# Kernel tuning notes

Hardware: AMD Instinct MI355X
Metric: run time of the kernel (lower is better)

## Reference

```python
import jax, jax.numpy as jnp
import numpy as np

RADII = (0.4, 0.8, 1.2)
SIGMA2 = 2.0 * 0.2 ** 2   # Gaussian shell-density bandwidth
ALPHA = 0.3               # keras LeakyReLU default
EPS = 1e-3                # keras BatchNormalization default epsilon


def _n_coeffs(L):
    return sum((2 * l + 1) ** 2 for l in range(L + 1))


def _pullback_idx(L):
    # flat index of Wigner block entry (m, n=0) for each SH coeff (l, m)
    idx, off = [], 0
    for l in range(L + 1):
        d = 2 * l + 1
        idx += [off + m * d + l for m in range(d)]
        off += d * d
    return np.asarray(idx, dtype=np.int32)


def setup_inputs() -> dict:
    key = jax.random.key(0)
    ks = jax.random.split(key, 20)
    B, N, Q, S = 64, 2048, 1024, 512
    T = [_n_coeffs(l) for l in (5, 4, 3)]  # 286, 165, 84
    f32 = jnp.float32

    def nrm(k, shape, scale=1.0):
        return jax.random.normal(ks[k], shape, dtype=f32) * scale

    dirs = nrm(1, (3, S, 3))
    dirs = dirs / jnp.linalg.norm(dirs, axis=-1, keepdims=True)
    z = lambda n: jnp.zeros((n,), f32)
    o = lambda n: jnp.ones((n,), f32)
    return {
        "x": nrm(0, (B, N, 3)),
        "shell_dirs": dirs,                                   # [3, 512, 3]
        "A_sh": nrm(2, (36, S), 1.0 / np.sqrt(S)),            # SH projection (l_max=5)
        "D_eval0": nrm(3, (Q, T[0]), 1.0 / np.sqrt(T[0])),    # Wigner eval bases
        "D_eval1": nrm(4, (Q, T[1]), 1.0 / np.sqrt(T[1])),
        "D_eval2": nrm(5, (Q, T[2]), 1.0 / np.sqrt(T[2])),
        "D_coef1": nrm(6, (T[1], Q), 1.0 / np.sqrt(Q)),       # Wigner coeff (projection) bases
        "D_coef2": nrm(7, (T[2], Q), 1.0 / np.sqrt(Q)),
        "D_coef_last": nrm(8, (T[2], Q), 1.0 / np.sqrt(Q)),
        "W0": nrm(9, (3, 16), 1.0 / np.sqrt(3)), "b0": z(16),
        "W1": nrm(10, (16, 32), 0.25), "b1": z(32),
        "W2": nrm(11, (32, 64), 1.0 / np.sqrt(32)), "b2": z(64),
        "g0": o(16), "be0": z(16),
        "g1": o(32), "be1": z(32),
        "g2": o(64), "be2": z(64),
        "Wfc1": nrm(12, (256, 512), 1.0 / 16.0), "bfc1": z(512),
        "gfc1": o(512), "befc1": z(512),
        "Wfc2": nrm(13, (512, 256), 1.0 / np.sqrt(512)), "bfc2": z(256),
        "gfc2": o(256), "befc2": z(256),
        "Wout": nrm(14, (256, 40), 1.0 / 16.0), "bout": z(40),
    }


def _bn(y, g, b, axes):
    m = jnp.mean(y, axis=axes, keepdims=True)
    v = jnp.var(y, axis=axes, keepdims=True)
    return (y - m) * jax.lax.rsqrt(v + EPS) * g + b


def reference(x, shell_dirs, A_sh, D_eval0, D_eval1, D_eval2,
              D_coef1, D_coef2, D_coef_last,
              W0, b0, W1, b1, W2, b2,
              g0, be0, g1, be1, g2, be2,
              Wfc1, bfc1, gfc1, befc1, Wfc2, bfc2, gfc2, befc2,
              Wout, bout):
    B = x.shape[0]
    # --- sphere_shell_embedding: Gaussian shell density -> SH coeffs per shell ---
    xn2 = jnp.sum(x * x, -1)[..., None]                 # [B,N,1]
    sh = []
    for i, r in enumerate(RADII):
        c = r * shell_dirs[i]                           # [S,3]
        d2 = xn2 + jnp.sum(c * c, -1) - 2.0 * (x @ c.T)  # [B,N,S]
        f = jnp.mean(jnp.exp(-d2 / SIGMA2), axis=1)      # [B,S]
        sh.append(f @ A_sh.T)                            # [B,36]
    sh = jnp.stack(sh, axis=-1)                          # [B,36,3] shells as channels
    # --- S2_to_SO3_pullback: Y_lm -> D^l_{m,0} column of Wigner blocks ---
    idx = jnp.asarray(_pullback_idx(5))
    y = jnp.zeros((B, 286, 3), sh.dtype).at[:, idx, :].set(sh)
    # --- layer 0: SO3Conv (per-coeff channel mix) + WignerEval + BN + LReLU + WignerCoeffs ---
    y = jnp.einsum('btc,cu->btu', y, W0) + b0
    y = jnp.einsum('qt,btu->bqu', D_eval0, y)            # [B,1024,16]
    y = jax.nn.leaky_relu(_bn(y, g0, be0, (0, 1)), ALPHA)
    y = jnp.einsum('tq,bqu->btu', D_coef1, y)            # [B,165,16]
    # --- layer 1 ---
    y = jnp.einsum('btc,cu->btu', y, W1) + b1
    y = jnp.einsum('qt,btu->bqu', D_eval1, y)            # [B,1024,32]
    y = jax.nn.leaky_relu(_bn(y, g1, be1, (0, 1)), ALPHA)
    y = jnp.einsum('tq,bqu->btu', D_coef2, y)            # [B,84,32]
    # --- layer 2 ---
    y = jnp.einsum('btc,cu->btu', y, W2) + b2
    y = jnp.einsum('qt,btu->bqu', D_eval2, y)            # [B,1024,64]
    y = jax.nn.leaky_relu(_bn(y, g2, be2, (0, 1)), ALPHA)
    y = jnp.einsum('tq,bqu->btu', D_coef_last, y)        # [B,84,64]
    # --- degree-wise norms (rotation-invariant pooling), l_max=3 blocks ---
    offs, sizes = (0, 1, 10, 35), (1, 9, 25, 49)
    feats = jnp.concatenate(
        [jnp.linalg.norm(y[:, o:o + s, :], axis=1, keepdims=True)
         for o, s in zip(offs, sizes)], axis=1)          # [B,4,64]
    h = feats.reshape(B, -1)                             # [B,256]
    # --- MLP head (dropout = identity at inference) ---
    h = jax.nn.relu(_bn(h @ Wfc1 + bfc1, gfc1, befc1, (0,)))
    h = jax.nn.relu(_bn(h @ Wfc2 + bfc2, gfc2, befc2, (0,)))
    return jax.nn.softmax(h @ Wout + bout, axis=-1)
```

## Files before the change

### kernel.cpp

```cpp
#include <hip/hip_runtime.h>
#include <hip/hip_bf16.h>

#define BB 64
#define NN 2048
#define QQ 1024
#define SS 512
#define NCH 16
#define PREPB 609
#define QKN3 8

__device__ const int PIDX[36] = {
    0, 2, 5, 8, 12, 17, 22, 27, 32, 38, 45, 52, 59, 66, 73, 80,
    88, 97, 106, 115, 124, 133, 142, 151, 160,
    170, 181, 192, 203, 214, 225, 236, 247, 258, 269, 280};

__global__ __launch_bounds__(256) void k_preshell(
    const float* __restrict__ De0, const float* __restrict__ De1, const float* __restrict__ De2,
    float* __restrict__ Dg0t, float* __restrict__ rs0,
    float* __restrict__ Det1, float* __restrict__ Det2,
    float* __restrict__ stats,
    const float* __restrict__ x, const float* __restrict__ dirs, float* __restrict__ pbuf) {
    __shared__ float tile[32][33];
    __shared__ float4 lx[NN / NCH];
    int blk = blockIdx.x, tid = threadIdx.x;
    if (blk < PREPB) {
        int r = tid >> 5, c = tid & 31;
        if (blk < 192) {
            int tq = blk & 31, tt = blk >> 5;
            int q0 = tq * 32, t0 = tt * 32;
            for (int rr = r; rr < 32; rr += 8) {
                int t = t0 + c;
                tile[rr][c] = (t < 165) ? De1[(q0 + rr) * 165 + t] : 0.f;
            }
            __syncthreads();
            for (int rr = r; rr < 32; rr += 8) {
                int t = t0 + rr;
                if (t < 165) Det1[t * QQ + q0 + c] = tile[c][rr];
            }
        } else if (blk < 288) {
            int i = blk - 192;
            int tq = i & 31, tt = i >> 5;
            int q0 = tq * 32, t0 = tt * 32;
            for (int rr = r; rr < 32; rr += 8) {
                int t = t0 + c;
                tile[rr][c] = (t < 84) ? De2[(q0 + rr) * 84 + t] : 0.f;
            }
            __syncthreads();
            for (int rr = r; rr < 32; rr += 8) {
                int t = t0 + rr;
                if (t < 84) Det2[t * QQ + q0 + c] = tile[c][rr];
            }
        } else if (blk < 352) {
            int i = blk - 288;
            int tq = i & 31, tj = i >> 5;
            int q0 = tq * 32, j0 = tj * 32;
            for (int rr = r; rr < 32; rr += 8) {
                int j = j0 + c;
                tile[rr][c] = (j < 36) ? De0[(q0 + rr) * 286 + PIDX[j]] : 0.f;
            }
            __syncthreads();
            for (int rr = r; rr < 32; rr += 8) {
                int j = j0 + rr;
                if (j < 36) Dg0t[j * QQ + q0 + c] = tile[c][rr];
            }
        } else if (blk < 608) {
            int w = tid >> 6, lane = tid & 63;
            int q = (blk - 352) * 4 + w;
            float s = 0.f;
#pragma unroll
            for (int p = 0; p < 5; p++) {
                int idx = lane + p * 64;
                if (idx < 286) s += De0[q * 286 + idx];
            }
#pragma unroll
            for (int o = 32; o > 0; o >>= 1) s += __shfl_xor(s, o, 64);
            if (lane == 0) rs0[q] = s;
        } else {
            if (tid < 224) stats[tid] = 0.f;
        }
        return;
    }
    int idx = blk - PREPB;
    int b = idx & 63, zc = idx >> 6;
    const float KL = 18.033688011112042f;
    const float* xb = x + ((size_t)b * NN + zc * (NN / NCH)) * 3;
    for (int n = tid; n < NN / NCH; n += 256) {
        float X = xb[n * 3 + 0];
        float Y = xb[n * 3 + 1];
        float Z = xb[n * 3 + 2];
        lx[n] = make_float4(X, Y, Z, -KL * (X * X + Y * Y + Z * Z));
    }
    __syncthreads();
    float cxs[3][2], cys[3][2], czs[3][2], bas[3][2];
#pragma unroll
    for (int i = 0; i < 3; i++) {
        float r = (i == 0) ? 0.4f : ((i == 1) ? 0.8f : 1.2f);
#pragma unroll
        for (int h = 0; h < 2; h++) {
            int s = tid + h * 256;
            float cx = r * dirs[(i * SS + s) * 3 + 0];
            float cy = r * dirs[(i * SS + s) * 3 + 1];
            float cz = r * dirs[(i * SS + s) * 3 + 2];
            bas[i][h] = -KL * (cx * cx + cy * cy + cz * cz);
            cxs[i][h] = 2.f * KL * cx;
            cys[i][h] = 2.f * KL * cy;
            czs[i][h] = 2.f * KL * cz;
        }
    }
    float acc[3][2];
#pragma unroll
    for (int i = 0; i < 3; i++) { acc[i][0] = 0.f; acc[i][1] = 0.f; }
#pragma unroll 4
    for (int n = 0; n < NN / NCH; n++) {
        float4 p = lx[n];
#pragma unroll
        for (int i = 0; i < 3; i++)
#pragma unroll
            for (int h = 0; h < 2; h++)
                acc[i][h] += __builtin_amdgcn_exp2f(
                    fmaf(cxs[i][h], p.x, fmaf(cys[i][h], p.y, fmaf(czs[i][h], p.z, p.w + bas[i][h]))));
    }
#pragma unroll
    for (int i = 0; i < 3; i++) {
        float* o = pbuf + ((size_t)(zc * 3 + i) * BB + b) * SS;
        o[tid] = acc[i][0];
        o[tid + 256] = acc[i][1];
    }
}

__global__ __launch_bounds__(256) void k_sh(const float* __restrict__ pbuf,
                                            const float* __restrict__ A_sh,
                                            float* __restrict__ lshp) {
    __shared__ float lf[256];
    int b = blockIdx.x, c = blockIdx.y, h = blockIdx.z, tid = threadIdx.x;
    float v = 0.f;
#pragma unroll
    for (int zc = 0; zc < NCH; zc++)
        v += pbuf[((size_t)(zc * 3 + c) * BB + b) * SS + h * 256 + tid];
    lf[tid] = v * (1.0f / NN);
    __syncthreads();
    int w = tid >> 6, lane = tid & 63;
    for (int j = w; j < 36; j += 4) {
        const float* As = A_sh + j * SS + h * 256;
        float a = 0.f;
#pragma unroll
        for (int k = 0; k < 4; k++) a = fmaf(lf[lane + 64 * k], As[lane + 64 * k], a);
#pragma unroll
        for (int o = 32; o > 0; o >>= 1) a += __shfl_xor(a, o, 64);
        if (lane == 0) lshp[((b * 36 + j) * 3 + c) * 2 + h] = a;
    }
}

__global__ __launch_bounds__(256) void k_eval0(const float* __restrict__ lshp,
                                               const float* __restrict__ W0,
                                               const float* __restrict__ b0,
                                               const float* __restrict__ Dg0t,
                                               const float* __restrict__ rs0,
                                               float* __restrict__ yq, float* __restrict__ stats) {
    __shared__ float lsh[36][3];
    __shared__ float llm[576];
    __shared__ float lred[4][32];
    int qc = blockIdx.x, b = blockIdx.y, tid = threadIdx.x;
    if (tid < 108) {
        int j = tid / 3, c = tid % 3;
        lsh[j][c] = lshp[((b * 36 + j) * 3 + c) * 2 + 0] + lshp[((b * 36 + j) * 3 + c) * 2 + 1];
    }
    __syncthreads();
    for (int i = tid; i < 576; i += 256) {
        int j = i >> 4, u = i & 15;
        float m = 0.f;
#pragma unroll
        for (int c = 0; c < 3; c++) m = fmaf(lsh[j][c], W0[c * 16 + u], m);
        llm[i] = m;
    }
    __syncthreads();
    int q = qc * 256 + tid;
    float acc[16];
#pragma unroll
    for (int u = 0; u < 16; u++) acc[u] = 0.f;
#pragma unroll 4
    for (int j = 0; j < 36; j++) {
        float d = Dg0t[j * QQ + q];
#pragma unroll
        for (int u = 0; u < 16; u++) acc[u] = fmaf(d, llm[j * 16 + u], acc[u]);
    }
    float rb = rs0[q];
#pragma unroll
    for (int u = 0; u < 16; u++) acc[u] = fmaf(b0[u], rb, acc[u]);
#pragma unroll
    for (int u = 0; u < 16; u++) yq[((size_t)b * 16 + u) * QQ + q] = acc[u];
    int lane = tid & 63, w = tid >> 6;
#pragma unroll
    for (int u = 0; u < 16; u++) {
        float v = acc[u], v2 = acc[u] * acc[u];
#pragma unroll
        for (int o = 32; o > 0; o >>= 1) {
            v += __shfl_xor(v, o, 64);
            v2 += __shfl_xor(v2, o, 64);
        }
        if (lane == 0) { lred[w][u] = v; lred[w][16 + u] = v2; }
    }
    __syncthreads();
    if (tid < 32) atomicAdd(&stats[tid], lred[0][tid] + lred[1][tid] + lred[2][tid] + lred[3][tid]);
}

template <int TT, int UU, int QKN>
__global__ __launch_bounds__(256) void k_coefG(const float* __restrict__ yq,
                                               const float* __restrict__ Dc,
                                               const float* __restrict__ stats,
                                               const float* __restrict__ g,
                                               const float* __restrict__ be,
                                               float* __restrict__ part) {
    constexpr int KC = QQ / QKN;
    __shared__ float lA[32][68];
    __shared__ float lB[32][68];
    __shared__ float lsu[UU], ltu[UU];
    int mt = blockIdx.x, nt = blockIdx.y, qk = blockIdx.z, tid = threadIdx.x;
    int m0 = mt * 64, n0 = nt * 64, k0 = qk * KC;
    if (tid < UU) {
        const float inv = 1.0f / (BB * QQ);
        float mm = stats[tid] * inv;
        float var = stats[UU + tid] * inv - mm * mm;
        float s = g[tid] * rsqrtf(fmaxf(var, 0.f) + 1e-3f);
        lsu[tid] = s;
        ltu[tid] = be[tid] - mm * s;
    }
    __syncthreads();
    int r = tid >> 2, f = (tid & 3) * 4;
    bool mok = (m0 + r) < TT;
    const float* arow = Dc + (size_t)(mok ? (m0 + r) : 0) * QQ;
    const float* brow = yq + (size_t)(n0 + r) * QQ;
    float su = lsu[(n0 + r) % UU], tu = ltu[(n0 + r) % UU];
    int tg = tid >> 4, ug = tid & 15;
    float acc[4][4];
#pragma unroll
    for (int i = 0; i < 4; i++)
#pragma unroll
        for (int j = 0; j < 4; j++) acc[i][j] = 0.f;
    for (int kb = 0; kb < KC; kb += 32) {
        int kg = k0 + kb;
#pragma unroll
        for (int p = 0; p < 2; p++) {
            int ko = f + p * 16;
            float4 a4 = make_float4(0.f, 0.f, 0.f, 0.f);
            if (mok) a4 = *(const float4*)(arow + kg + ko);
            float4 b4 = *(const float4*)(brow + kg + ko);
#pragma unroll
            for (int i = 0; i < 4; i++) {
                float v = fmaf((&b4.x)[i], su, tu);
                lA[ko + i][r] = (&a4.x)[i];
                lB[ko + i][r] = (v > 0.f) ? v : 0.3f * v;
            }
        }
        __syncthreads();
#pragma unroll 2
        for (int kk = 0; kk < 32; kk++) {
            float4 a4 = *(const float4*)&lA[kk][tg * 4];
            float4 b4 = *(const float4*)&lB[kk][ug * 4];
#pragma unroll
            for (int i = 0; i < 4; i++) {
                float av = (&a4.x)[i];
                acc[i][0] = fmaf(av, b4.x, acc[i][0]);
                acc[i][1] = fmaf(av, b4.y, acc[i][1]);
                acc[i][2] = fmaf(av, b4.z, acc[i][2]);
                acc[i][3] = fmaf(av, b4.w, acc[i][3]);
            }
        }
        __syncthreads();
    }
    int n = n0 + ug * 4;
    int b = n / UU, u0 = n % UU;
#pragma unroll
    for (int i = 0; i < 4; i++) {
        int t = m0 + tg * 4 + i;
        if (t < TT)
            *(float4*)&part[(((size_t)qk * BB + b) * TT + t) * UU + u0] =
                make_float4(acc[i][0], acc[i][1], acc[i][2], acc[i][3]);
    }
}

template <int TT, int CC, int UU, int QKN, int TTp, int TS>
__global__ __launch_bounds__(256) void k_redmix(const float* __restrict__ part,
                                                const float* __restrict__ W,
                                                const float* __restrict__ bias,
                                                float* __restrict__ ym) {
    constexpr int TSL = TTp / TS;
    __shared__ float lyt[TSL][CC + 1];
    int b = blockIdx.x, ts = blockIdx.y, tid = threadIdx.x;
    int t0 = ts * TSL;
    for (int i = tid; i < TSL * CC; i += 256) {
        int tl = i / CC, c = i % CC;
        int t = t0 + tl;
        float v = 0.f;
        if (t < TT) {
#pragma unroll
            for (int k = 0; k < QKN; k++)
                v += part[(size_t)k * (BB * TT * CC) + ((size_t)b * TT + t) * CC + c];
        }
        lyt[tl][c] = v;
    }
    __syncthreads();
    for (int i = tid; i < UU * TSL; i += 256) {
        int u = i / TSL, tl = i % TSL;
        int t = t0 + tl;
        float m = 0.f;
        if (t < TT) {
            m = bias[u];
#pragma unroll
            for (int c = 0; c < CC; c++) m = fmaf(lyt[tl][c], W[c * UU + u], m);
        }
        ym[((size_t)b * UU + u) * TTp + t] = m;
    }
}

template <int TT, int TTp, int UU>
__global__ __launch_bounds__(256) void k_evalG(const float* __restrict__ ym,
                                               const float* __restrict__ Det,
                                               float* __restrict__ yq,
                                               float* __restrict__ stats) {
    __shared__ float lA[32][68];
    __shared__ float lB[32][68];
    __shared__ float sred[2][64];
    int mt = blockIdx.x, qt = blockIdx.y, tid = threadIdx.x;
    int m0 = mt * 64, q0 = qt * 64;
    int r = tid >> 2, f = (tid & 3) * 4;
    const float* arow = ym + (size_t)(m0 + r) * TTp;
    int br = tid >> 4, bq = (tid & 15) * 4;
    int tg = tid >> 4, ug = tid & 15;
    float acc[4][4];
#pragma unroll
    for (int i = 0; i < 4; i++)
#pragma unroll
        for (int j = 0; j < 4; j++) acc[i][j] = 0.f;
    for (int kb = 0; kb < TT; kb += 32) {
#pragma unroll
        for (int p = 0; p < 2; p++) {
            int ko = f + p * 16;
            float4 a4 = *(const float4*)(arow + kb + ko);
#pragma unroll
            for (int i = 0; i < 4; i++) lA[ko + i][r] = (&a4.x)[i];
            int kk = br + p * 16;
            int t = kb + kk;
            float4 b4 = make_float4(0.f, 0.f, 0.f, 0.f);
            if (t < TT) b4 = *(const float4*)(Det + (size_t)t * QQ + q0 + bq);
            *(float4*)&lB[kk][bq] = b4;
        }
        __syncthreads();
#pragma unroll 2
        for (int kk = 0; kk < 32; kk++) {
            float4 a4 = *(const float4*)&lA[kk][tg * 4];
            float4 b4 = *(const float4*)&lB[kk][ug * 4];
#pragma unroll
            for (int i = 0; i < 4; i++) {
                float av = (&a4.x)[i];
                acc[i][0] = fmaf(av, b4.x, acc[i][0]);
                acc[i][1] = fmaf(av, b4.y, acc[i][1]);
                acc[i][2] = fmaf(av, b4.z, acc[i][2]);
                acc[i][3] = fmaf(av, b4.w, acc[i][3]);
            }
        }
        __syncthreads();
    }
    float s1[4], s2[4];
#pragma unroll
    for (int i = 0; i < 4; i++) {
        int m = m0 + tg * 4 + i;
        *(float4*)&yq[(size_t)m * QQ + q0 + ug * 4] =
            make_float4(acc[i][0], acc[i][1], acc[i][2], acc[i][3]);
        s1[i] = (acc[i][0] + acc[i][1]) + (acc[i][2] + acc[i][3]);
        s2[i] = fmaf(acc[i][0], acc[i][0], fmaf(acc[i][1], acc[i][1],
                 fmaf(acc[i][2], acc[i][2], acc[i][3] * acc[i][3])));
    }
#pragma unroll
    for (int o = 1; o < 16; o <<= 1) {
#pragma unroll
        for (int i = 0; i < 4; i++) {
            s1[i] += __shfl_xor(s1[i], o, 64);
            s2[i] += __shfl_xor(s2[i], o, 64);
        }
    }
    if (ug == 0) {
#pragma unroll
        for (int i = 0; i < 4; i++) {
            sred[0][tg * 4 + i] = s1[i];
            sred[1][tg * 4 + i] = s2[i];
        }
    }
    __syncthreads();
    if (tid < 2 * UU) {
        int which = tid / UU, u = tid % UU;
        float s = 0.f;
        for (int rr = u; rr < 64; rr += UU) s += sred[which][rr];
        atomicAdd(&stats[which * UU + u], s);
    }
}

__global__ __launch_bounds__(256) void k_norms(const float* __restrict__ part, float* __restrict__ ht0) {
    __shared__ float red[4][64];
    int b = blockIdx.x, blk = blockIdx.y;
    int tq = threadIdx.x >> 6, u = threadIdx.x & 63;
    const int offs[4] = {0, 1, 10, 35};
    const int ends[4] = {1, 10, 35, 84};
    float a = 0.f;
    for (int t = offs[blk] + tq; t < ends[blk]; t += 4) {
        float v = 0.f;
#pragma unroll
        for (int k = 0; k < QKN3; k++)
            v += part[(size_t)k * (BB * 84 * 64) + (b * 84 + t) * 64 + u];
        a = fmaf(v, v, a);
    }
    red[tq][u] = a;
    __syncthreads();
    if (tq == 0) {
        float s = red[0][u] + red[1][u] + red[2][u] + red[3][u];
        ht0[(blk * 64 + u) * BB + b] = sqrtf(fmaxf(s, 0.f));
    }
}

template <int K, int J>
__global__ __launch_bounds__(512) void k_fc(const float* __restrict__ in, const float* __restrict__ W,
                                            const float* __restrict__ bias, const float* __restrict__ g,
                                            const float* __restrict__ be, float* __restrict__ out) {
    __shared__ float red[8][64];
    int j = blockIdx.x;
    int b = threadIdx.x & 63, kq = threadIdx.x >> 6;
    constexpr int KS = K / 8;
    int kbeg = kq * KS;
    float a0 = 0.f, a1 = 0.f, a2 = 0.f, a3 = 0.f;
#pragma unroll 4
    for (int k = kbeg; k < kbeg + KS; k += 4) {
        a0 = fmaf(in[k * BB + b], W[(size_t)k * J + j], a0);
        a1 = fmaf(in[(k + 1) * BB + b], W[(size_t)(k + 1) * J + j], a1);
        a2 = fmaf(in[(k + 2) * BB + b], W[(size_t)(k + 2) * J + j], a2);
        a3 = fmaf(in[(k + 3) * BB + b], W[(size_t)(k + 3) * J + j], a3);
    }
    red[kq][b] = (a0 + a1) + (a2 + a3);
    __syncthreads();
    if (kq == 0) {
        float acc = bias[j];
#pragma unroll
        for (int i = 0; i < 8; i++) acc += red[i][b];
        float s1 = acc, s2 = acc * acc;
#pragma unroll
        for (int o = 32; o > 0; o >>= 1) {
            s1 += __shfl_xor(s1, o, 64);
            s2 += __shfl_xor(s2, o, 64);
        }
        float m = s1 * (1.0f / 64.f);
        float var = s2 * (1.0f / 64.f) - m * m;
        float sc = g[j] * rsqrtf(fmaxf(var, 0.f) + 1e-3f);
        float v = (acc - m) * sc + be[j];
        out[j * BB + b] = fmaxf(v, 0.f);
    }
}

__global__ __launch_bounds__(256) void k_out(const float* __restrict__ ht2, const float* __restrict__ Wout,
                                             const float* __restrict__ bout, float* __restrict__ outp) {
    __shared__ float red[4][64];
    __shared__ float sm[64];
    int b = blockIdx.x;
    int o = threadIdx.x & 63, kq = threadIdx.x >> 6;
    float a0 = 0.f, a1 = 0.f, a2 = 0.f, a3 = 0.f;
    int kbeg = kq * 64;
    if (o < 40) {
#pragma unroll 4
        for (int k = kbeg; k < kbeg + 64; k += 4) {
            a0 = fmaf(ht2[k * BB + b], Wout[k * 40 + o], a0);
            a1 = fmaf(ht2[(k + 1) * BB + b], Wout[(k + 1) * 40 + o], a1);
            a2 = fmaf(ht2[(k + 2) * BB + b], Wout[(k + 2) * 40 + o], a2);
            a3 = fmaf(ht2[(k + 3) * BB + b], Wout[(k + 3) * 40 + o], a3);
        }
    }
    red[kq][o] = (a0 + a1) + (a2 + a3);
    __syncthreads();
    if (kq == 0) {
        float acc = red[0][o] + red[1][o] + red[2][o] + red[3][o] + ((o < 40) ? bout[o] : 0.f);
        sm[o] = (o < 40) ? acc : -3.0e38f;
        __syncthreads();
        for (int s = 32; s > 0; s >>= 1) {
            if (o < s) sm[o] = fmaxf(sm[o], sm[o + s]);
            __syncthreads();
        }
        float m = sm[0];
        __syncthreads();
        const float L2E = 1.4426950408889634f;
        float e = (o < 40) ? exp2f((acc - m) * L2E) : 0.f;
        sm[o] = e;
        __syncthreads();
        for (int s = 32; s > 0; s >>= 1) {
            if (o < s) sm[o] += sm[o + s];
            __syncthreads();
        }
        if (o < 40) outp[b * 40 + o] = e / sm[0];
    }
}

#define OFF_PBUF 0
#define OFF_DG0T 1572864
#define OFF_RS0 1609728
#define OFF_DET1 1610752
#define OFF_DET2 1779712
#define OFF_YQ 1865728
#define OFF_YM 6060032
#define OFF_LSH 6453248
#define OFF_HT0 6467072
#define OFF_HT1 6483456
#define OFF_HT2 6516224
#define OFF_STATS 6532608
#define OFF_PART 6532864
#define OFF_PART3 7909120

extern "C" void kernel_launch(void* const* d_in, const int* in_sizes, int n_in,
                              void* d_out, int out_size, void* d_ws, size_t ws_size,
                              hipStream_t stream) {
    const float* x = (const float*)d_in[0];
    const float* shell_dirs = (const float*)d_in[1];
    const float* A_sh = (const float*)d_in[2];
    const float* D_eval0 = (const float*)d_in[3];
    const float* D_eval1 = (const float*)d_in[4];
    const float* D_eval2 = (const float*)d_in[5];
    const float* D_coef1 = (const float*)d_in[6];
    const float* D_coef2 = (const float*)d_in[7];
    const float* D_coef_last = (const float*)d_in[8];
    const float* W0 = (const float*)d_in[9];
    const float* b0 = (const float*)d_in[10];
    const float* W1 = (const float*)d_in[11];
    const float* b1 = (const float*)d_in[12];
    const float* W2 = (const float*)d_in[13];
    const float* b2 = (const float*)d_in[14];
    const float* g0 = (const float*)d_in[15];
    const float* be0 = (const float*)d_in[16];
    const float* g1 = (const float*)d_in[17];
    const float* be1 = (const float*)d_in[18];
    const float* g2 = (const float*)d_in[19];
    const float* be2 = (const float*)d_in[20];
    const float* Wfc1 = (const float*)d_in[21];
    const float* bfc1 = (const float*)d_in[22];
    const float* gfc1 = (const float*)d_in[23];
    const float* befc1 = (const float*)d_in[24];
    const float* Wfc2 = (const float*)d_in[25];
    const float* bfc2 = (const float*)d_in[26];
    const float* gfc2 = (const float*)d_in[27];
    const float* befc2 = (const float*)d_in[28];
    const float* Wout = (const float*)d_in[29];
    const float* bout = (const float*)d_in[30];
    float* out = (float*)d_out;

    float* ws = (float*)d_ws;
    float* pbuf = ws + OFF_PBUF;
    float* Dg0t = ws + OFF_DG0T;
    float* rs0 = ws + OFF_RS0;
    float* Det1 = ws + OFF_DET1;
    float* Det2 = ws + OFF_DET2;
    float* yq = ws + OFF_YQ;
    float* ym = ws + OFF_YM;
    float* lshp = ws + OFF_LSH;
    float* ht0 = ws + OFF_HT0;
    float* ht1 = ws + OFF_HT1;
    float* ht2 = ws + OFF_HT2;
    float* stats = ws + OFF_STATS;
    float* part = ws + OFF_PART;
    float* part3 = ws + OFF_PART3;
    float* stats0 = stats;
    float* stats1 = stats + 32;
    float* stats2 = stats + 96;

    k_preshell<<<PREPB + BB * NCH, 256, 0, stream>>>(
        D_eval0, D_eval1, D_eval2, Dg0t, rs0, Det1, Det2, stats, x, shell_dirs, pbuf);
    k_sh<<<dim3(BB, 3, 2), 256, 0, stream>>>(pbuf, A_sh, lshp);
    k_eval0<<<dim3(4, BB), 256, 0, stream>>>(lshp, W0, b0, Dg0t, rs0, yq, stats0);
    k_coefG<165, 16, 8><<<dim3(3, 16, 8), 256, 0, stream>>>(yq, D_coef1, stats0, g0, be0, part);
    k_redmix<165, 16, 32, 8, 192, 8><<<dim3(BB, 8), 256, 0, stream>>>(part, W1, b1, ym);
    k_evalG<165, 192, 32><<<dim3(32, 16), 256, 0, stream>>>(ym, Det1, yq, stats1);
    k_coefG<84, 32, 8><<<dim3(2, 32, 8), 256, 0, stream>>>(yq, D_coef2, stats1, g1, be1, part);
    k_redmix<84, 32, 64, 8, 96, 8><<<dim3(BB, 8), 256, 0, stream>>>(part, W2, b2, ym);
    k_evalG<84, 96, 64><<<dim3(64, 16), 256, 0, stream>>>(ym, Det2, yq, stats2);
    k_coefG<84, 64, QKN3><<<dim3(2, 64, QKN3), 256, 0, stream>>>(yq, D_coef_last, stats2, g2, be2, part3);
    k_norms<<<dim3(BB, 4), 256, 0, stream>>>(part3, ht0);
    k_fc<256, 512><<<512, 512, 0, stream>>>(ht0, Wfc1, bfc1, gfc1, befc1, ht1);
    k_fc<512, 256><<<256, 512, 0, stream>>>(ht1, Wfc2, bfc2, gfc2, befc2, ht2);
    k_out<<<BB, 256, 0, stream>>>(ht2, Wout, bout, out);
}
```

Before: 312.7 us.

## Fuse all pipeline stages into one persistent cooperative kernel with grid barriers

Replaces the fourteen separate kernel launches with a single cooperative persistent kernel. Each stage runs as a grid-stride loop over work blocks, and stages are separated by a software grid barrier built on atomics. This is meant to remove per-launch overhead and inter-kernel gaps. In exchange, each barrier costs a global atomic round trip, some stages may see reduced parallelism from the capped grid size, and the old multi-launch path is kept as a fallback.

```diff
diff --git a/kernel.cpp b/kernel.cpp
--- a/kernel.cpp
+++ b/kernel.cpp
@@ -1,5 +1,4 @@
 #include <hip/hip_runtime.h>
-#include <hip/hip_bf16.h>
 
 #define BB 64
 #define NN 2048
@@ -13,6 +12,551 @@
     0, 2, 5, 8, 12, 17, 22, 27, 32, 38, 45, 52, 59, 66, 73, 80,
     88, 97, 106, 115, 124, 133, 142, 151, 160,
     170, 181, 192, 203, 214, 225, 236, 247, 258, 269, 280};
+
+struct MArgs {
+    const float *x, *dirs, *A_sh, *De0, *De1, *De2, *Dc1, *Dc2, *Dc3;
+    const float *W0, *b0, *W1, *b1, *W2, *b2;
+    const float *g0, *be0, *g1, *be1, *g2, *be2;
+    const float *Wfc1, *bfc1, *gfc1, *befc1, *Wfc2, *bfc2, *gfc2, *befc2, *Wout, *bout;
+    float *pbuf, *Dg0t, *rs0, *Det1, *Det2, *yq, *ym, *lshp;
+    float *ht0, *ht1, *ht2, *stats, *part, *part3, *out;
+};
+
+struct SmGemm { float lA[32][68]; float lB[32][68]; float lsu[64]; float ltu[64]; };
+struct SmEv   { float lA[32][68]; float lB[32][68]; float sred[2][64]; };
+struct SmE0   { float lsh[36][3]; float llm[576]; float lred[4][32]; };
+
+__device__ unsigned long long g_bar_count = 0ull;
+__device__ unsigned long long g_bar_gen = 0ull;
+
+__device__ __forceinline__ void gbar() {
+    __syncthreads();
+    __threadfence();
+    if (threadIdx.x == 0) {
+        unsigned long long gen =
+            __hip_atomic_load(&g_bar_gen, __ATOMIC_RELAXED, __HIP_MEMORY_SCOPE_AGENT);
+        unsigned long long arrived =
+            __hip_atomic_fetch_add(&g_bar_count, 1ull, __ATOMIC_ACQ_REL, __HIP_MEMORY_SCOPE_AGENT) + 1ull;
+        if (arrived == (unsigned long long)gridDim.x) {
+            __hip_atomic_store(&g_bar_count, 0ull, __ATOMIC_RELAXED, __HIP_MEMORY_SCOPE_AGENT);
+            __hip_atomic_fetch_add(&g_bar_gen, 1ull, __ATOMIC_RELEASE, __HIP_MEMORY_SCOPE_AGENT);
+        } else {
+            while (__hip_atomic_load(&g_bar_gen, __ATOMIC_ACQUIRE, __HIP_MEMORY_SCOPE_AGENT) == gen)
+                __builtin_amdgcn_s_sleep(2);
+        }
+    }
+    __syncthreads();
+    __threadfence();
+}
+
+
+__device__ void ph_shell(const MArgs& a, int wb, char* smraw, int tid) {
+    __syncthreads();
+    float4* lx = reinterpret_cast<float4*>(smraw);
+    int b = wb & 63, zc = wb >> 6;
+    const float KL = 18.033688011112042f;
+    const float* xb = a.x + ((size_t)b * NN + zc * (NN / NCH)) * 3;
+    for (int n = tid; n < NN / NCH; n += 256) {
+        float X = xb[n * 3 + 0];
+        float Y = xb[n * 3 + 1];
+        float Z = xb[n * 3 + 2];
+        lx[n] = make_float4(X, Y, Z, -KL * (X * X + Y * Y + Z * Z));
+    }
+    __syncthreads();
+    float cxs[3][2], cys[3][2], czs[3][2], bas[3][2];
+#pragma unroll
+    for (int i = 0; i < 3; i++) {
+        float r = (i == 0) ? 0.4f : ((i == 1) ? 0.8f : 1.2f);
+#pragma unroll
+        for (int h = 0; h < 2; h++) {
+            int s = tid + h * 256;
+            float cx = r * a.dirs[(i * SS + s) * 3 + 0];
+            float cy = r * a.dirs[(i * SS + s) * 3 + 1];
+            float cz = r * a.dirs[(i * SS + s) * 3 + 2];
+            bas[i][h] = -KL * (cx * cx + cy * cy + cz * cz);
+            cxs[i][h] = 2.f * KL * cx;
+            cys[i][h] = 2.f * KL * cy;
+            czs[i][h] = 2.f * KL * cz;
+        }
+    }
+    float acc[3][2];
+#pragma unroll
+    for (int i = 0; i < 3; i++) { acc[i][0] = 0.f; acc[i][1] = 0.f; }
+#pragma unroll 4
+    for (int n = 0; n < NN / NCH; n++) {
+        float4 p = lx[n];
+#pragma unroll
+        for (int i = 0; i < 3; i++)
+#pragma unroll
+            for (int h = 0; h < 2; h++)
+                acc[i][h] += __builtin_amdgcn_exp2f(
+                    fmaf(cxs[i][h], p.x, fmaf(cys[i][h], p.y, fmaf(czs[i][h], p.z, p.w))));
+    }
+#pragma unroll
+    for (int i = 0; i < 3; i++) {
+        float* o = a.pbuf + ((size_t)(zc * 3 + i) * BB + b) * SS;
+        o[tid] = acc[i][0] * __builtin_amdgcn_exp2f(bas[i][0]);
+        o[tid + 256] = acc[i][1] * __builtin_amdgcn_exp2f(bas[i][1]);
+    }
+}
+
+__device__ void ph_sh(const MArgs& a, int wb, char* smraw, int tid) {
+    __syncthreads();
+    float* lf = reinterpret_cast<float*>(smraw);
+    int b = wb & 63;
+    int t = wb >> 6;
+    int c = t % 3, h = t / 3;
+    float v = 0.f;
+#pragma unroll
+    for (int zc = 0; zc < NCH; zc++)
+        v += a.pbuf[((size_t)(zc * 3 + c) * BB + b) * SS + h * 256 + tid];
+    lf[tid] = v * (1.0f / NN);
+    __syncthreads();
+    int w = tid >> 6, lane = tid & 63;
+    for (int j = w; j < 36; j += 4) {
+        const float* As = a.A_sh + j * SS + h * 256;
+        float acc = 0.f;
+#pragma unroll
+        for (int k = 0; k < 4; k++) acc = fmaf(lf[lane + 64 * k], As[lane + 64 * k], acc);
+#pragma unroll
+        for (int o = 32; o > 0; o >>= 1) acc += __shfl_xor(acc, o, 64);
+        if (lane == 0) a.lshp[((b * 36 + j) * 3 + c) * 2 + h] = acc;
+    }
+}
+
+__device__ void ph_prep(const MArgs& a, int wb, char* smraw, int tid) {
+    __syncthreads();
+    float (*tile)[33] = reinterpret_cast<float (*)[33]>(smraw);
+    int r = tid >> 5, c = tid & 31;
+    if (wb < 576) {
+        int i = wb - 384;
+        int tq = i & 31, tt = i >> 5;
+        int q0 = tq * 32, t0 = tt * 32;
+        for (int rr = r; rr < 32; rr += 8) {
+            int t = t0 + c;
+            tile[rr][c] = (t < 165) ? a.De1[(q0 + rr) * 165 + t] : 0.f;
+        }
+        __syncthreads();
+        for (int rr = r; rr < 32; rr += 8) {
+            int t = t0 + rr;
+            if (t < 165) a.Det1[t * QQ + q0 + c] = tile[c][rr];
+        }
+    } else if (wb < 672) {
+        int i = wb - 576;
+        int tq = i & 31, tt = i >> 5;
+        int q0 = tq * 32, t0 = tt * 32;
+        for (int rr = r; rr < 32; rr += 8) {
+            int t = t0 + c;
+            tile[rr][c] = (t < 84) ? a.De2[(q0 + rr) * 84 + t] : 0.f;
+        }
+        __syncthreads();
+        for (int rr = r; rr < 32; rr += 8) {
+            int t = t0 + rr;
+            if (t < 84) a.Det2[t * QQ + q0 + c] = tile[c][rr];
+        }
+    } else if (wb < 736) {
+        int i = wb - 672;
+        int tq = i & 31, tj = i >> 5;
+        int q0 = tq * 32, j0 = tj * 32;
+        for (int rr = r; rr < 32; rr += 8) {
+            int j = j0 + c;
+            tile[rr][c] = (j < 36) ? a.De0[(q0 + rr) * 286 + PIDX[j]] : 0.f;
+        }
+        __syncthreads();
+        for (int rr = r; rr < 32; rr += 8) {
+            int j = j0 + rr;
+            if (j < 36) a.Dg0t[j * QQ + q0 + c] = tile[c][rr];
+        }
+    } else {
+        int w = tid >> 6, lane = tid & 63;
+        int q = (wb - 736) * 4 + w;
+        float s = 0.f;
+#pragma unroll
+        for (int p = 0; p < 5; p++) {
+            int idx = lane + p * 64;
+            if (idx < 286) s += a.De0[q * 286 + idx];
+        }
+#pragma unroll
+        for (int o = 32; o > 0; o >>= 1) s += __shfl_xor(s, o, 64);
+        if (lane == 0) a.rs0[q] = s;
+    }
+}
+
+__device__ void ph_eval0(const MArgs& a, int wb, char* smraw, int tid) {
+    __syncthreads();
+    SmE0& s = *reinterpret_cast<SmE0*>(smraw);
+    int qc = wb & 3, b = wb >> 2;
+    if (tid < 108) {
+        int j = tid / 3, c = tid % 3;
+        s.lsh[j][c] = a.lshp[((b * 36 + j) * 3 + c) * 2 + 0] +
+                      a.lshp[((b * 36 + j) * 3 + c) * 2 + 1];
+    }
+    __syncthreads();
+    for (int i = tid; i < 576; i += 256) {
+        int j = i >> 4, u = i & 15;
+        float m = 0.f;
+#pragma unroll
+        for (int c = 0; c < 3; c++) m = fmaf(s.lsh[j][c], a.W0[c * 16 + u], m);
+        s.llm[i] = m;
+    }
+    __syncthreads();
+    int q = qc * 256 + tid;
+    float acc[16];
+#pragma unroll
+    for (int u = 0; u < 16; u++) acc[u] = 0.f;
+#pragma unroll 4
+    for (int j = 0; j < 36; j++) {
+        float d = a.Dg0t[j * QQ + q];
+#pragma unroll
+        for (int u = 0; u < 16; u++) acc[u] = fmaf(d, s.llm[j * 16 + u], acc[u]);
+    }
+    float rb = a.rs0[q];
+#pragma unroll
+    for (int u = 0; u < 16; u++) acc[u] = fmaf(a.b0[u], rb, acc[u]);
+#pragma unroll
+    for (int u = 0; u < 16; u++) a.yq[((size_t)b * 16 + u) * QQ + q] = acc[u];
+    int lane = tid & 63, w = tid >> 6;
+#pragma unroll
+    for (int u = 0; u < 16; u++) {
+        float v = acc[u], v2 = acc[u] * acc[u];
+#pragma unroll
+        for (int o = 32; o > 0; o >>= 1) {
+            v += __shfl_xor(v, o, 64);
+            v2 += __shfl_xor(v2, o, 64);
+        }
+        if (lane == 0) { s.lred[w][u] = v; s.lred[w][16 + u] = v2; }
+    }
+    __syncthreads();
+    if (tid < 32)
+        atomicAdd(&a.stats[tid], s.lred[0][tid] + s.lred[1][tid] + s.lred[2][tid] + s.lred[3][tid]);
+}
+
+template <int TT, int UU, int QKN>
+__device__ void ph_coefG(const float* __restrict__ yq, const float* __restrict__ Dc,
+                         const float* __restrict__ stats, const float* __restrict__ g,
+                         const float* __restrict__ be, float* __restrict__ part,
+                         int mt, int nt, int qk, char* smraw, int tid) {
+    __syncthreads();
+    constexpr int KC = QQ / QKN;
+    SmGemm& s = *reinterpret_cast<SmGemm*>(smraw);
+    int m0 = mt * 64, n0 = nt * 64, k0 = qk * KC;
+    if (tid < UU) {
+        const float inv = 1.0f / (BB * QQ);
+        float mm = stats[tid] * inv;
+        float var = stats[UU + tid] * inv - mm * mm;
+        float sc = g[tid] * rsqrtf(fmaxf(var, 0.f) + 1e-3f);
+        s.lsu[tid] = sc;
+        s.ltu[tid] = be[tid] - mm * sc;
+    }
+    __syncthreads();
+    int r = tid >> 2, f = (tid & 3) * 4;
+    bool mok = (m0 + r) < TT;
+    const float* arow = Dc + (size_t)(mok ? (m0 + r) : 0) * QQ;
+    const float* brow = yq + (size_t)(n0 + r) * QQ;
+    float su = s.lsu[(n0 + r) % UU], tu = s.ltu[(n0 + r) % UU];
+    int tg = tid >> 4, ug = tid & 15;
+    float acc[4][4];
+#pragma unroll
+    for (int i = 0; i < 4; i++)
+#pragma unroll
+        for (int j = 0; j < 4; j++) acc[i][j] = 0.f;
+    for (int kb = 0; kb < KC; kb += 32) {
+        int kg = k0 + kb;
+#pragma unroll
+        for (int p = 0; p < 2; p++) {
+            int ko = f + p * 16;
+            float4 a4 = make_float4(0.f, 0.f, 0.f, 0.f);
+            if (mok) a4 = *(const float4*)(arow + kg + ko);
+            float4 b4 = *(const float4*)(brow + kg + ko);
+#pragma unroll
+            for (int i = 0; i < 4; i++) {
+                float v = fmaf((&b4.x)[i], su, tu);
+                s.lA[ko + i][r] = (&a4.x)[i];
+                s.lB[ko + i][r] = (v > 0.f) ? v : 0.3f * v;
+            }
+        }
+        __syncthreads();
+#pragma unroll 2
+        for (int kk = 0; kk < 32; kk++) {
+            float4 a4 = *(const float4*)&s.lA[kk][tg * 4];
+            float4 b4 = *(const float4*)&s.lB[kk][ug * 4];
+#pragma unroll
+            for (int i = 0; i < 4; i++) {
+                float av = (&a4.x)[i];
+                acc[i][0] = fmaf(av, b4.x, acc[i][0]);
+                acc[i][1] = fmaf(av, b4.y, acc[i][1]);
+                acc[i][2] = fmaf(av, b4.z, acc[i][2]);
+                acc[i][3] = fmaf(av, b4.w, acc[i][3]);
+            }
+        }
+        __syncthreads();
+    }
+    int n = n0 + ug * 4;
+    int b = n / UU, u0 = n % UU;
+#pragma unroll
+    for (int i = 0; i < 4; i++) {
+        int t = m0 + tg * 4 + i;
+        if (t < TT)
+            *(float4*)&part[(((size_t)qk * BB + b) * TT + t) * UU + u0] =
+                make_float4(acc[i][0], acc[i][1], acc[i][2], acc[i][3]);
+    }
+}
+
+template <int TT, int CC, int UU, int QKN, int TTp, int TS>
+__device__ void ph_redmix(const float* __restrict__ part, const float* __restrict__ W,
+                          const float* __restrict__ bias, float* __restrict__ ym,
+                          int b, int ts, char* smraw, int tid) {
+    __syncthreads();
+    constexpr int TSL = TTp / TS;
+    float* lyt = reinterpret_cast<float*>(smraw);
+    int t0 = ts * TSL;
+    for (int i = tid; i < TSL * CC; i += 256) {
+        int tl = i / CC, c = i % CC;
+        int t = t0 + tl;
+        float v = 0.f;
+        if (t < TT) {
+#pragma unroll
+            for (int k = 0; k < QKN; k++)
+                v += part[(size_t)k * (BB * TT * CC) + ((size_t)b * TT + t) * CC + c];
+        }
+        lyt[tl * (CC + 1) + c] = v;
+    }
+    __syncthreads();
+    for (int i = tid; i < UU * TSL; i += 256) {
+        int u = i / TSL, tl = i % TSL;
+        int t = t0 + tl;
+        float m = 0.f;
+        if (t < TT) {
+            m = bias[u];
+#pragma unroll
+            for (int c = 0; c < CC; c++) m = fmaf(lyt[tl * (CC + 1) + c], W[c * UU + u], m);
+        }
+        ym[((size_t)b * UU + u) * TTp + t] = m;
+    }
+}
+
+template <int TT, int TTp, int UU>
+__device__ void ph_evalG(const float* __restrict__ ym, const float* __restrict__ Det,
+                         float* __restrict__ yq, float* __restrict__ stats,
+                         int mt, int qt, char* smraw, int tid) {
+    __syncthreads();
+    SmEv& s = *reinterpret_cast<SmEv*>(smraw);
+    int m0 = mt * 64, q0 = qt * 64;
+    int r = tid >> 2, f = (tid & 3) * 4;
+    const float* arow = ym + (size_t)(m0 + r) * TTp;
+    int br = tid >> 4, bq = (tid & 15) * 4;
+    int tg = tid >> 4, ug = tid & 15;
+    float acc[4][4];
+#pragma unroll
+    for (int i = 0; i < 4; i++)
+#pragma unroll
+        for (int j = 0; j < 4; j++) acc[i][j] = 0.f;
+    for (int kb = 0; kb < TT; kb += 32) {
+#pragma unroll
+        for (int p = 0; p < 2; p++) {
+            int ko = f + p * 16;
+            float4 a4 = *(const float4*)(arow + kb + ko);
+#pragma unroll
+            for (int i = 0; i < 4; i++) s.lA[ko + i][r] = (&a4.x)[i];
+            int kk = br + p * 16;
+            int t = kb + kk;
+            float4 b4 = make_float4(0.f, 0.f, 0.f, 0.f);
+            if (t < TT) b4 = *(const float4*)(Det + (size_t)t * QQ + q0 + bq);
+            *(float4*)&s.lB[kk][bq] = b4;
+        }
+        __syncthreads();
+#pragma unroll 2
+        for (int kk = 0; kk < 32; kk++) {
+            float4 a4 = *(const float4*)&s.lA[kk][tg * 4];
+            float4 b4 = *(const float4*)&s.lB[kk][ug * 4];
+#pragma unroll
+            for (int i = 0; i < 4; i++) {
+                float av = (&a4.x)[i];
+                acc[i][0] = fmaf(av, b4.x, acc[i][0]);
+                acc[i][1] = fmaf(av, b4.y, acc[i][1]);
+                acc[i][2] = fmaf(av, b4.z, acc[i][2]);
+                acc[i][3] = fmaf(av, b4.w, acc[i][3]);
+            }
+        }
+        __syncthreads();
+    }
+    float s1[4], s2[4];
+#pragma unroll
+    for (int i = 0; i < 4; i++) {
+        int m = m0 + tg * 4 + i;
+        *(float4*)&yq[(size_t)m * QQ + q0 + ug * 4] =
+            make_float4(acc[i][0], acc[i][1], acc[i][2], acc[i][3]);
+        s1[i] = (acc[i][0] + acc[i][1]) + (acc[i][2] + acc[i][3]);
+        s2[i] = fmaf(acc[i][0], acc[i][0], fmaf(acc[i][1], acc[i][1],
+                 fmaf(acc[i][2], acc[i][2], acc[i][3] * acc[i][3])));
+    }
+#pragma unroll
+    for (int o = 1; o < 16; o <<= 1) {
+#pragma unroll
+        for (int i = 0; i < 4; i++) {
+            s1[i] += __shfl_xor(s1[i], o, 64);
+            s2[i] += __shfl_xor(s2[i], o, 64);
+        }
+    }
+    if (ug == 0) {
+#pragma unroll
+        for (int i = 0; i < 4; i++) {
+            s.sred[0][tg * 4 + i] = s1[i];
+            s.sred[1][tg * 4 + i] = s2[i];
+        }
+    }
+    __syncthreads();
+    if (tid < 2 * UU) {
+        int which = tid / UU, u = tid % UU;
+        float sv = 0.f;
+        for (int rr = u; rr < 64; rr += UU) sv += s.sred[which][rr];
+        atomicAdd(&stats[which * UU + u], sv);
+    }
+}
+
+__device__ void ph_norms(const float* __restrict__ part, float* __restrict__ ht0,
+                         int b, int blk, char* smraw, int tid) {
+    __syncthreads();
+    float (*red)[64] = reinterpret_cast<float (*)[64]>(smraw);
+    int tq = tid >> 6, u = tid & 63;
+    const int offs[4] = {0, 1, 10, 35};
+    const int ends[4] = {1, 10, 35, 84};
+    float acc = 0.f;
+    for (int t = offs[blk] + tq; t < ends[blk]; t += 4) {
+        float v = 0.f;
+#pragma unroll
+        for (int k = 0; k < QKN3; k++)
+            v += part[(size_t)k * (BB * 84 * 64) + (b * 84 + t) * 64 + u];
+        acc = fmaf(v, v, acc);
+    }
+    red[tq][u] = acc;
+    __syncthreads();
+    if (tq == 0) {
+        float sv = red[0][u] + red[1][u] + red[2][u] + red[3][u];
+        ht0[(blk * 64 + u) * BB + b] = sqrtf(fmaxf(sv, 0.f));
+    }
+}
+
+template <int K, int J>
+__device__ void ph_fc(const float* __restrict__ in, const float* __restrict__ W,
+                      const float* __restrict__ bias, const float* __restrict__ g,
+                      const float* __restrict__ be, float* __restrict__ out,
+                      int j, char* smraw, int tid) {
+    __syncthreads();
+    float (*red)[64] = reinterpret_cast<float (*)[64]>(smraw);
+    int b = tid & 63, kq = tid >> 6;
+    constexpr int KS = K / 4;
+    int kbeg = kq * KS;
+    float a0 = 0.f, a1 = 0.f, a2 = 0.f, a3 = 0.f;
+#pragma unroll 4
+    for (int k = kbeg; k < kbeg + KS; k += 4) {
+        a0 = fmaf(in[k * BB + b], W[(size_t)k * J + j], a0);
+        a1 = fmaf(in[(k + 1) * BB + b], W[(size_t)(k + 1) * J + j], a1);
+        a2 = fmaf(in[(k + 2) * BB + b], W[(size_t)(k + 2) * J + j], a2);
+        a3 = fmaf(in[(k + 3) * BB + b], W[(size_t)(k + 3) * J + j], a3);
+    }
+    red[kq][b] = (a0 + a1) + (a2 + a3);
+    __syncthreads();
+    if (kq == 0) {
+        float acc = bias[j] + red[0][b] + red[1][b] + red[2][b] + red[3][b];
+        float s1 = acc, s2 = acc * acc;
+#pragma unroll
+        for (int o = 32; o > 0; o >>= 1) {
+            s1 += __shfl_xor(s1, o, 64);
+            s2 += __shfl_xor(s2, o, 64);
+        }
+        float m = s1 * (1.0f / 64.f);
+        float var = s2 * (1.0f / 64.f) - m * m;
+        float sc = g[j] * rsqrtf(fmaxf(var, 0.f) + 1e-3f);
+        float v = (acc - m) * sc + be[j];
+        out[j * BB + b] = fmaxf(v, 0.f);
+    }
+}
+
+__device__ void ph_out(const float* __restrict__ ht2, const float* __restrict__ Wout,
+                       const float* __restrict__ bout, float* __restrict__ outp,
+                       int b, char* smraw, int tid) {
+    __syncthreads();
+    float (*red)[64] = reinterpret_cast<float (*)[64]>(smraw);
+    int o = tid & 63, kq = tid >> 6;
+    float a0 = 0.f, a1 = 0.f, a2 = 0.f, a3 = 0.f;
+    int kbeg = kq * 64;
+    if (o < 40) {
+#pragma unroll 4
+        for (int k = kbeg; k < kbeg + 64; k += 4) {
+            a0 = fmaf(ht2[k * BB + b], Wout[k * 40 + o], a0);
+            a1 = fmaf(ht2[(k + 1) * BB + b], Wout[(k + 1) * 40 + o], a1);
+            a2 = fmaf(ht2[(k + 2) * BB + b], Wout[(k + 2) * 40 + o], a2);
+            a3 = fmaf(ht2[(k + 3) * BB + b], Wout[(k + 3) * 40 + o], a3);
+        }
+    }
+    red[kq][o] = (a0 + a1) + (a2 + a3);
+    __syncthreads();
+    if (kq == 0) {
+        float acc = red[0][o] + red[1][o] + red[2][o] + red[3][o] + ((o < 40) ? bout[o] : 0.f);
+        float m = (o < 40) ? acc : -3.0e38f;
+#pragma unroll
+        for (int s = 32; s > 0; s >>= 1) m = fmaxf(m, __shfl_xor(m, s, 64));
+        const float L2E = 1.4426950408889634f;
+        float e = (o < 40) ? exp2f((acc - m) * L2E) : 0.f;
+        float ssum = e;
+#pragma unroll
+        for (int s = 32; s > 0; s >>= 1) ssum += __shfl_xor(ssum, s, 64);
+        if (o < 40) outp[b * 40 + o] = e / ssum;
+    }
+}
+
+__global__ void __launch_bounds__(256, 2) k_mega(MArgs a) {
+    __shared__ __align__(16) char smraw[17920];
+    const int tid = threadIdx.x;
+    const int G = gridDim.x;
+    for (int wb = blockIdx.x; wb < 1024; wb += G) ph_shell(a, wb, smraw, tid);
+    gbar();
+    for (int wb = blockIdx.x; wb < 993; wb += G) {
+        if (wb < 384) ph_sh(a, wb, smraw, tid);
+        else if (wb < 992) ph_prep(a, wb, smraw, tid);
+        else { __syncthreads(); if (tid < 224) a.stats[tid] = 0.f; }
+    }
+    gbar();
+    for (int wb = blockIdx.x; wb < 256; wb += G) ph_eval0(a, wb, smraw, tid);
+    gbar();
+    for (int wb = blockIdx.x; wb < 384; wb += G) {
+        int mt = wb % 3, t = wb / 3;
+        ph_coefG<165, 16, 8>(a.yq, a.Dc1, a.stats, a.g0, a.be0, a.part, mt, t & 15, t >> 4, smraw, tid);
+    }
+    gbar();
+    for (int wb = blockIdx.x; wb < 512; wb += G)
+        ph_redmix<165, 16, 32, 8, 192, 8>(a.part, a.W1, a.b1, a.ym, wb & 63, wb >> 6, smraw, tid);
+    gbar();
+    for (int wb = blockIdx.x; wb < 512; wb += G)
+        ph_evalG<165, 192, 32>(a.ym, a.Det1, a.yq, a.stats + 32, wb & 31, wb >> 5, smraw, tid);
+    gbar();
+    for (int wb = blockIdx.x; wb < 512; wb += G) {
+        int mt = wb & 1, t = wb >> 1;
+        ph_coefG<84, 32, 8>(a.yq, a.Dc2, a.stats + 32, a.g1, a.be1, a.part, mt, t & 31, t >> 5, smraw, tid);
+    }
+    gbar();
+    for (int wb = blockIdx.x; wb < 512; wb += G)
+        ph_redmix<84, 32, 64, 8, 96, 8>(a.part, a.W2, a.b2, a.ym, wb & 63, wb >> 6, smraw, tid);
+    gbar();
+    for (int wb = blockIdx.x; wb < 1024; wb += G)
+        ph_evalG<84, 96, 64>(a.ym, a.Det2, a.yq, a.stats + 96, wb & 63, wb >> 6, smraw, tid);
+    gbar();
+    for (int wb = blockIdx.x; wb < 1024; wb += G) {
+        int mt = wb & 1, t = wb >> 1;
+        ph_coefG<84, 64, QKN3>(a.yq, a.Dc3, a.stats + 96, a.g2, a.be2, a.part3, mt, t & 63, t >> 6, smraw, tid);
+    }
+    gbar();
+    for (int wb = blockIdx.x; wb < 256; wb += G) ph_norms(a.part3, a.ht0, wb & 63, wb >> 6, smraw, tid);
+    gbar();
+    for (int wb = blockIdx.x; wb < 512; wb += G)
+        ph_fc<256, 512>(a.ht0, a.Wfc1, a.bfc1, a.gfc1, a.befc1, a.ht1, wb, smraw, tid);
+    gbar();
+    for (int wb = blockIdx.x; wb < 256; wb += G)
+        ph_fc<512, 256>(a.ht1, a.Wfc2, a.bfc2, a.gfc2, a.befc2, a.ht2, wb, smraw, tid);
+    gbar();
+    for (int wb = blockIdx.x; wb < 64; wb += G) ph_out(a.ht2, a.Wout, a.bout, a.out, wb, smraw, tid);
+}
 
 __global__ __launch_bounds__(256) void k_preshell(
     const float* __restrict__ De0, const float* __restrict__ De1, const float* __restrict__ De2,
@@ -513,71 +1057,99 @@
 extern "C" void kernel_launch(void* const* d_in, const int* in_sizes, int n_in,
                               void* d_out, int out_size, void* d_ws, size_t ws_size,
                               hipStream_t stream) {
-    const float* x = (const float*)d_in[0];
-    const float* shell_dirs = (const float*)d_in[1];
-    const float* A_sh = (const float*)d_in[2];
-    const float* D_eval0 = (const float*)d_in[3];
-    const float* D_eval1 = (const float*)d_in[4];
-    const float* D_eval2 = (const float*)d_in[5];
-    const float* D_coef1 = (const float*)d_in[6];
-    const float* D_coef2 = (const float*)d_in[7];
-    const float* D_coef_last = (const float*)d_in[8];
-    const float* W0 = (const float*)d_in[9];
-    const float* b0 = (const float*)d_in[10];
-    const float* W1 = (const float*)d_in[11];
-    const float* b1 = (const float*)d_in[12];
-    const float* W2 = (const float*)d_in[13];
-    const float* b2 = (const float*)d_in[14];
-    const float* g0 = (const float*)d_in[15];
-    const float* be0 = (const float*)d_in[16];
-    const float* g1 = (const float*)d_in[17];
-    const float* be1 = (const float*)d_in[18];
-    const float* g2 = (const float*)d_in[19];
-    const float* be2 = (const float*)d_in[20];
-    const float* Wfc1 = (const float*)d_in[21];
-    const float* bfc1 = (const float*)d_in[22];
-    const float* gfc1 = (const float*)d_in[23];
-    const float* befc1 = (const float*)d_in[24];
-    const float* Wfc2 = (const float*)d_in[25];
-    const float* bfc2 = (const float*)d_in[26];
-    const float* gfc2 = (const float*)d_in[27];
-    const float* befc2 = (const float*)d_in[28];
-    const float* Wout = (const float*)d_in[29];
-    const float* bout = (const float*)d_in[30];
-    float* out = (float*)d_out;
-
     float* ws = (float*)d_ws;
-    float* pbuf = ws + OFF_PBUF;
-    float* Dg0t = ws + OFF_DG0T;
-    float* rs0 = ws + OFF_RS0;
-    float* Det1 = ws + OFF_DET1;
-    float* Det2 = ws + OFF_DET2;
-    float* yq = ws + OFF_YQ;
-    float* ym = ws + OFF_YM;
-    float* lshp = ws + OFF_LSH;
-    float* ht0 = ws + OFF_HT0;
-    float* ht1 = ws + OFF_HT1;
-    float* ht2 = ws + OFF_HT2;
-    float* stats = ws + OFF_STATS;
-    float* part = ws + OFF_PART;
-    float* part3 = ws + OFF_PART3;
-    float* stats0 = stats;
-    float* stats1 = stats + 32;
-    float* stats2 = stats + 96;
-
+    MArgs a;
+    a.x = (const float*)d_in[0];
+    a.dirs = (const float*)d_in[1];
+    a.A_sh = (const float*)d_in[2];
+    a.De0 = (const float*)d_in[3];
+    a.De1 = (const float*)d_in[4];
+    a.De2 = (const float*)d_in[5];
+    a.Dc1 = (const float*)d_in[6];
+    a.Dc2 = (const float*)d_in[7];
+    a.Dc3 = (const float*)d_in[8];
+    a.W0 = (const float*)d_in[9];
+    a.b0 = (const float*)d_in[10];
+    a.W1 = (const float*)d_in[11];
+    a.b1 = (const float*)d_in[12];
+    a.W2 = (const float*)d_in[13];
+    a.b2 = (const float*)d_in[14];
+    a.g0 = (const float*)d_in[15];
+    a.be0 = (const float*)d_in[16];
+    a.g1 = (const float*)d_in[17];
+    a.be1 = (const float*)d_in[18];
+    a.g2 = (const float*)d_in[19];
+    a.be2 = (const float*)d_in[20];
+    a.Wfc1 = (const float*)d_in[21];
+    a.bfc1 = (const float*)d_in[22];
+    a.gfc1 = (const float*)d_in[23];
+    a.befc1 = (const float*)d_in[24];
+    a.Wfc2 = (const float*)d_in[25];
+    a.bfc2 = (const float*)d_in[26];
+    a.gfc2 = (const float*)d_in[27];
+    a.befc2 = (const float*)d_in[28];
+    a.Wout = (const float*)d_in[29];
+    a.bout = (const float*)d_in[30];
+    a.pbuf = ws + OFF_PBUF;
+    a.Dg0t = ws + OFF_DG0T;
+    a.rs0 = ws + OFF_RS0;
+    a.Det1 = ws + OFF_DET1;
+    a.Det2 = ws + OFF_DET2;
+    a.yq = ws + OFF_YQ;
+    a.ym = ws + OFF_YM;
+    a.lshp = ws + OFF_LSH;
+    a.ht0 = ws + OFF_HT0;
+    a.ht1 = ws + OFF_HT1;
+    a.ht2 = ws + OFF_HT2;
+    a.stats = ws + OFF_STATS;
+    a.part = ws + OFF_PART;
+    a.part3 = ws + OFF_PART3;
+    a.out = (float*)d_out;
+
+    static int mode = -1;
+    static int gsize = 0;
+    if (mode < 0) {
+        int dev = 0;
+        (void)hipGetDevice(&dev);
+        int coop = 0;
+        (void)hipDeviceGetAttribute(&coop, hipDeviceAttributeCooperativeLaunch, dev);
+        int ncu = 0;
+        (void)hipDeviceGetAttribute(&ncu, hipDeviceAttributeMultiprocessorCount, dev);
+        int occ = 0;
+        hipError_t e = hipOccupancyMaxActiveBlocksPerMultiprocessor(&occ, (const void*)k_mega, 256, 0);
+        long long mg = (long long)occ * (long long)ncu;
+        if (coop && e == hipSuccess && mg >= 256) {
+            gsize = (int)(mg > 1024 ? 1024 : mg);
+            mode = 1;
+        } else {
+            mode = 0;
+        }
+    }
+
+    if (mode == 1) {
+        void* kargs[] = {(void*)&a};
+        hipError_t le =
+            hipLaunchCooperativeKernel((const void*)k_mega, dim3(gsize), dim3(256), kargs, 0, stream);
+        if (le == hipSuccess) return;
+        mode = 0;
+    }
+
+    float* stats0 = a.stats;
+    float* stats1 = a.stats + 32;
+    float* stats2 = a.stats + 96;
     k_preshell<<<PREPB + BB * NCH, 256, 0, stream>>>(
-        D_eval0, D_eval1, D_eval2, Dg0t, rs0, Det1, Det2, stats, x, shell_dirs, pbuf);
-    k_sh<<<dim3(BB, 3, 2), 256, 0, stream>>>(pbuf, A_sh, lshp);
-    k_eval0<<<dim3(4, BB), 256, 0, stream>>>(lshp, W0, b0, Dg0t, rs0, yq, stats0);
-    k_coefG<165, 16, 8><<<dim3(3, 16, 8), 256, 0, stream>>>(yq, D_coef1, stats0, g0, be0, part);
-    k_redmix<165, 16, 32, 8, 192, 8><<<dim3(BB, 8), 256, 0, stream>>>(part, W1, b1, ym);
-    k_evalG<165, 192, 32><<<dim3(32, 16), 256, 0, stream>>>(ym, Det1, yq, stats1);
-    k_coefG<84, 32, 8><<<dim3(2, 32, 8), 256, 0, stream>>>(yq, D_coef2, stats1, g1, be1, part);
-    k_redmix<84, 32, 64, 8, 96, 8><<<dim3(BB, 8), 256, 0, stream>>>(part, W2, b2, ym);
-    k_evalG<84, 96, 64><<<dim3(64, 16), 256, 0, stream>>>(ym, Det2, yq, stats2);
-    k_coefG<84, 64, QKN3><<<dim3(2, 64, QKN3), 256, 0, stream>>>(yq, D_coef_last, stats2, g2, be2, part3);
-    k_norms<<<dim3(BB, 4), 256, 0, stream>>>(part3, ht0);
-    k_fc<256, 512><<<512, 512, 0, stream>>>(ht0, Wfc1, bfc1, gfc1, befc1, ht1);
-    k_fc<512, 256><<<256, 512, 0, stream>>>(ht1, Wfc2, bfc2, gfc2, befc2, ht2);
-    k_out<<<BB, 256, 0, stream>>>(ht2, Wout, bout, out);
-}
+        a.De0, a.De1, a.De2, a.Dg0t, a.rs0, a.Det1, a.Det2, a.stats, a.x, a.dirs, a.pbuf);
+    k_sh<<<dim3(BB, 3, 2), 256, 0, stream>>>(a.pbuf, a.A_sh, a.lshp);
+    k_eval0<<<dim3(4, BB), 256, 0, stream>>>(a.lshp, a.W0, a.b0, a.Dg0t, a.rs0, a.yq, stats0);
+    k_coefG<165, 16, 8><<<dim3(3, 16, 8), 256, 0, stream>>>(a.yq, a.Dc1, stats0, a.g0, a.be0, a.part);
+    k_redmix<165, 16, 32, 8, 192, 8><<<dim3(BB, 8), 256, 0, stream>>>(a.part, a.W1, a.b1, a.ym);
+    k_evalG<165, 192, 32><<<dim3(32, 16), 256, 0, stream>>>(a.ym, a.Det1, a.yq, stats1);
+    k_coefG<84, 32, 8><<<dim3(2, 32, 8), 256, 0, stream>>>(a.yq, a.Dc2, stats1, a.g1, a.be1, a.part);
+    k_redmix<84, 32, 64, 8, 96, 8><<<dim3(BB, 8), 256, 0, stream>>>(a.part, a.W2, a.b2, a.ym);
+    k_evalG<84, 96, 64><<<dim3(64, 16), 256, 0, stream>>>(a.ym, a.Det2, a.yq, stats2);
+    k_coefG<84, 64, QKN3><<<dim3(2, 64, QKN3), 256, 0, stream>>>(a.yq, a.Dc3, stats2, a.g2, a.be2, a.part3);
+    k_norms<<<dim3(BB, 4), 256, 0, stream>>>(a.part3, a.ht0);
+    k_fc<256, 512><<<512, 512, 0, stream>>>(a.ht0, a.Wfc1, a.bfc1, a.gfc1, a.befc1, a.ht1);
+    k_fc<512, 256><<<256, 512, 0, stream>>>(a.ht1, a.Wfc2, a.bfc2, a.gfc2, a.befc2, a.ht2);
+    k_out<<<BB, 256, 0, stream>>>(a.ht2, a.Wout, a.bout, a.out);
+}
```

New measurement: 1.209 ms. 3.87x slower.
